# Performance work log

Measured on AMD Instinct MI355X. Metric: run time of the kernel, lower is better.

The kernel has to match this reference:

```python
import jax, jax.numpy as jnp
import numpy as np

N_CLASSES = 19
N_BINS = 10
EPS = 1e-13


def setup_inputs() -> dict:
    key = jax.random.key(0)
    k1, k2 = jax.random.split(key)
    output = jax.random.normal(k1, (1, N_CLASSES, 1024, 2048), dtype=jnp.float32)
    target = jax.random.randint(k2, (1, 1024, 2048), 0, N_CLASSES, dtype=jnp.int32)
    return {"output": output, "target": target}


def reference(output, target):
    # output: [B, C, H, W] logits; target: [B, H, W] int labels
    B, C, H, W = output.shape
    p = jax.nn.softmax(output, axis=1)  # [B, C, H, W]

    # Bin i covers (i/N_BINS, (i+1)/N_BINS]; p == 0 belongs to no bin.
    bin_idx = jnp.clip(jnp.ceil(p * N_BINS).astype(jnp.int32) - 1, 0, N_BINS - 1)
    valid = p > 0

    cls = jnp.arange(C, dtype=jnp.int32)[None, :, None, None]  # idealMap per class
    # Combined (class, bin) segment id; invalid pixels dumped into extra segment.
    seg = jnp.where(valid, cls * N_BINS + bin_idx, C * N_BINS).reshape(-1)
    n_seg = C * N_BINS + 1

    p_flat = p.reshape(-1)
    conf_sum = jax.ops.segment_sum(p_flat, seg, num_segments=n_seg)[:-1].reshape(C, N_BINS)
    no_pred = jax.ops.segment_sum(jnp.ones_like(p_flat), seg, num_segments=n_seg)[:-1].reshape(C, N_BINS)
    correct = (target[:, None, :, :] == cls).astype(p.dtype)  # idealMap == target
    no_acc = jax.ops.segment_sum(correct.reshape(-1), seg, num_segments=n_seg)[:-1].reshape(C, N_BINS)

    avg_acc = no_acc / (no_pred + EPS)
    avg_conf = conf_sum / (no_pred + EPS)
    loss = jnp.sum((avg_acc - avg_conf) ** 2 * (no_pred / jnp.sum(no_pred)))
    return loss
```

## Files before the change

### kernel.cpp

```cpp
#include <hip/hip_runtime.h>

#define NC 19
#define NB 10
#define NCELL (NC * NB)
#define NPART (3 * NCELL + 2 * NC)
#define REP 16
#define NSLOT 32
#define TPB 256
#define BLOCKS 768

typedef float f32x4 __attribute__((ext_vector_type(4)));

__global__ __launch_bounds__(TPB, 3) void cce_pass1(
    const float* __restrict__ logits, const int* __restrict__ tgt,
    float* __restrict__ gacc, int hw)
{
    constexpr int O_CONF = 0;
    constexpr int O_PRED = REP * NCELL;
    constexpr int O_ACC  = 2 * REP * NCELL;
    constexpr int O_PSUM = 3 * REP * NCELL;
    constexpr int O_INV  = O_PSUM + REP * NC;
    constexpr int LDS_N  = O_INV + NC;

    __shared__ float hist[LDS_N];
    for (int i = threadIdx.x; i < LDS_N; i += TPB) hist[i] = 0.0f;
    __syncthreads();

    const int rep = threadIdx.x & (REP - 1);
    float psum[NC];
#pragma unroll
    for (int c = 0; c < NC; ++c) psum[c] = 0.0f;

    const int ngr      = hw >> 2;
    const int tid      = blockIdx.x * TPB + threadIdx.x;
    const int nthreads = (int)gridDim.x * TPB;

    for (int g = tid; g < ngr; g += nthreads) {
        const unsigned voff = (unsigned)g * 16u;
        f32x4 xv[19];
#define LD(i) asm volatile("global_load_dwordx4 %0, %1, %2"                      \
                           : "=v"(xv[i])                                          \
                           : "v"(voff), "s"(logits + (size_t)(i) * hw));
        LD(0) LD(1) LD(2) LD(3) LD(4) LD(5) LD(6) LD(7) LD(8) LD(9)
        LD(10) LD(11) LD(12) LD(13) LD(14) LD(15) LD(16) LD(17) LD(18)
#undef LD
        const int4 tq = *reinterpret_cast<const int4*>(tgt + 4 * (size_t)g);
        asm volatile("s_waitcnt vmcnt(0)"
                     : "+v"(xv[0]), "+v"(xv[1]), "+v"(xv[2]), "+v"(xv[3]),
                       "+v"(xv[4]), "+v"(xv[5]), "+v"(xv[6]), "+v"(xv[7]),
                       "+v"(xv[8]), "+v"(xv[9]), "+v"(xv[10]), "+v"(xv[11]),
                       "+v"(xv[12]), "+v"(xv[13]), "+v"(xv[14]), "+v"(xv[15]),
                       "+v"(xv[16]), "+v"(xv[17]), "+v"(xv[18])
                     :: "memory");

#pragma unroll
        for (int k = 0; k < 4; ++k) {
            const int tgk = (k == 0) ? tq.x : (k == 1) ? tq.y : (k == 2) ? tq.z : tq.w;

            float m = xv[0][k];
#pragma unroll
            for (int c = 1; c < NC; ++c) m = fmaxf(m, xv[c][k]);
            float s = 0.0f;
#pragma unroll
            for (int c = 0; c < NC; ++c) { xv[c][k] = __expf(xv[c][k] - m); s += xv[c][k]; }
            const float r = __builtin_amdgcn_rcpf(s);

            float pt = 0.0f, pmin = 1.0f;
#pragma unroll
            for (int c = 0; c < NC; ++c) {
                const float p = xv[c][k] * r;
                psum[c] += p;
                pt   = (c == tgk) ? p : pt;
                pmin = fminf(pmin, p);
                int bb = (int)ceilf(p * 10.0f) - 1;
                if (bb > 0) {
                    bb = bb > NB - 1 ? NB - 1 : bb;
                    atomicAdd(&hist[O_CONF + rep * NCELL + c * NB + bb], p);
                    atomicAdd(&hist[O_PRED + rep * NCELL + c * NB + bb], 1.0f);
                }
            }
            if (pt > 0.0f) {
                int bt = (int)ceilf(pt * 10.0f) - 1;
                bt = bt < 0 ? 0 : (bt > NB - 1 ? NB - 1 : bt);
                atomicAdd(&hist[O_ACC + rep * NCELL + tgk * NB + bt], 1.0f);
            }
            if (!(pmin > 0.0f)) {
#pragma unroll
                for (int c = 0; c < NC; ++c)
                    if (!(xv[c][k] * r > 0.0f)) atomicAdd(&hist[O_INV + c], 1.0f);
            }
        }
    }

#pragma unroll
    for (int c = 0; c < NC; ++c)
        atomicAdd(&hist[O_PSUM + rep * NC + c], psum[c]);
    __syncthreads();

    float* slot = gacc + (size_t)(blockIdx.x & (NSLOT - 1)) * NPART;
    for (int j = threadIdx.x; j < NPART; j += TPB) {
        float v = 0.0f;
        if (j < NCELL) {
            for (int rr = 0; rr < REP; ++rr) v += hist[O_CONF + rr * NCELL + j];
        } else if (j < 2 * NCELL) {
            for (int rr = 0; rr < REP; ++rr) v += hist[O_PRED + rr * NCELL + (j - NCELL)];
        } else if (j < 3 * NCELL) {
            for (int rr = 0; rr < REP; ++rr) v += hist[O_ACC + rr * NCELL + (j - 2 * NCELL)];
        } else if (j < 3 * NCELL + NC) {
            for (int rr = 0; rr < REP; ++rr) v += hist[O_PSUM + rr * NC + (j - 3 * NCELL)];
        } else {
            v = hist[O_INV + (j - 3 * NCELL - NC)];
        }
        atomicAdd(&slot[j], v);
    }
}

__global__ void cce_pass2(const float* __restrict__ gacc, float* __restrict__ out, int hw)
{
    __shared__ double fin[NPART];
    const int j = threadIdx.x;
    if (j < NPART) {
        double v = 0.0;
        for (int s = 0; s < NSLOT; ++s) v += (double)gacc[(size_t)s * NPART + j];
        fin[j] = v;
    }
    __syncthreads();

    if (j < NC) {
        double spred = 0.0, sconf = 0.0;
        for (int b = 1; b < NB; ++b) {
            spred += fin[NCELL + j * NB + b];
            sconf += fin[j * NB + b];
        }
        const double validc = (double)hw - fin[3 * NCELL + NC + j];
        fin[NCELL + j * NB] = validc - spred;
        fin[j * NB]         = fin[3 * NCELL + j] - sconf;
    }
    __syncthreads();

    if (j < 64) {
        double tot = 0.0;
        for (int c = j; c < NCELL; c += 64) tot += fin[NCELL + c];
#pragma unroll
        for (int o = 32; o > 0; o >>= 1) tot += __shfl_down(tot, o);
        tot = __shfl(tot, 0);

        double loss = 0.0;
        for (int c = j; c < NCELL; c += 64) {
            const double pred = fin[NCELL + c];
            const double conf = fin[c];
            const double acc  = fin[2 * NCELL + c];
            const double d    = (acc - conf) / (pred + 1e-13);
            loss += d * d * (pred / tot);
        }
#pragma unroll
        for (int o = 32; o > 0; o >>= 1) loss += __shfl_down(loss, o);
        if (j == 0) out[0] = (float)loss;
    }
}

extern "C" void kernel_launch(void* const* d_in, const int* in_sizes, int n_in,
                              void* d_out, int out_size, void* d_ws, size_t ws_size,
                              hipStream_t stream)
{
    const float* logits = (const float*)d_in[0];
    const int*   tgt    = (const int*)d_in[1];
    float*       gacc   = (float*)d_ws;
    const int    hw     = in_sizes[1];

    hipMemsetAsync(gacc, 0, (size_t)NSLOT * NPART * sizeof(float), stream);
    cce_pass1<<<BLOCKS, TPB, 0, stream>>>(logits, tgt, gacc, hw);
    cce_pass2<<<1, 640, 0, stream>>>(gacc, (float*)d_out, hw);
}
```

Measured before the change: 267.7 us.

## Process fixed 8-pixel chunk per thread with three-pass streaming softmax

Replaces the grid-stride loop, which held all 19 class vectors in registers, with a one-shot layout: each block covers 2048 pixels and each thread 8 pixels. The thread reads the logits three times (max, sum of exponentials, then histogram), relying on cache hits for the second and third reads so that fewer registers are live. Occupancy rises to 4 blocks per CU, and the LDS histogram replicas drop from 16 to 4 to save shared memory, which adds atomic contention. The grid is hardcoded to 1024 blocks with no bounds check, so the kernel only works when hw is exactly 1024*2048.

```diff
diff --git a/kernel.cpp b/kernel.cpp
--- a/kernel.cpp
+++ b/kernel.cpp
@@ -4,14 +4,16 @@
 #define NB 10
 #define NCELL (NC * NB)
 #define NPART (3 * NCELL + 2 * NC)
-#define REP 16
+#define REP 4
+#define REP16 16
 #define NSLOT 32
 #define TPB 256
-#define BLOCKS 768
+#define CHUNK 2048
+#define BLOCKS 1024
 
 typedef float f32x4 __attribute__((ext_vector_type(4)));
 
-__global__ __launch_bounds__(TPB, 3) void cce_pass1(
+__global__ __launch_bounds__(TPB, 4) void cce_pass1(
     const float* __restrict__ logits, const int* __restrict__ tgt,
     float* __restrict__ gacc, int hw)
 {
@@ -19,82 +21,88 @@
     constexpr int O_PRED = REP * NCELL;
     constexpr int O_ACC  = 2 * REP * NCELL;
     constexpr int O_PSUM = 3 * REP * NCELL;
-    constexpr int O_INV  = O_PSUM + REP * NC;
+    constexpr int O_INV  = O_PSUM + REP16 * NC;
     constexpr int LDS_N  = O_INV + NC;
 
     __shared__ float hist[LDS_N];
     for (int i = threadIdx.x; i < LDS_N; i += TPB) hist[i] = 0.0f;
     __syncthreads();
 
-    const int rep = threadIdx.x & (REP - 1);
-    float psum[NC];
+    const int rep   = threadIdx.x & (REP - 1);
+    const int rep16 = threadIdx.x & (REP16 - 1);
+    const size_t px0 = (size_t)blockIdx.x * CHUNK + (size_t)threadIdx.x * 8;
+
+    int tg[8];
+    {
+        const int4 t0 = *reinterpret_cast<const int4*>(tgt + px0);
+        const int4 t1 = *reinterpret_cast<const int4*>(tgt + px0 + 4);
+        tg[0]=t0.x; tg[1]=t0.y; tg[2]=t0.z; tg[3]=t0.w;
+        tg[4]=t1.x; tg[5]=t1.y; tg[6]=t1.z; tg[7]=t1.w;
+    }
+
+    float m[8];
 #pragma unroll
-    for (int c = 0; c < NC; ++c) psum[c] = 0.0f;
-
-    const int ngr      = hw >> 2;
-    const int tid      = blockIdx.x * TPB + threadIdx.x;
-    const int nthreads = (int)gridDim.x * TPB;
-
-    for (int g = tid; g < ngr; g += nthreads) {
-        const unsigned voff = (unsigned)g * 16u;
-        f32x4 xv[19];
-#define LD(i) asm volatile("global_load_dwordx4 %0, %1, %2"                      \
-                           : "=v"(xv[i])                                          \
-                           : "v"(voff), "s"(logits + (size_t)(i) * hw));
-        LD(0) LD(1) LD(2) LD(3) LD(4) LD(5) LD(6) LD(7) LD(8) LD(9)
-        LD(10) LD(11) LD(12) LD(13) LD(14) LD(15) LD(16) LD(17) LD(18)
-#undef LD
-        const int4 tq = *reinterpret_cast<const int4*>(tgt + 4 * (size_t)g);
-        asm volatile("s_waitcnt vmcnt(0)"
-                     : "+v"(xv[0]), "+v"(xv[1]), "+v"(xv[2]), "+v"(xv[3]),
-                       "+v"(xv[4]), "+v"(xv[5]), "+v"(xv[6]), "+v"(xv[7]),
-                       "+v"(xv[8]), "+v"(xv[9]), "+v"(xv[10]), "+v"(xv[11]),
-                       "+v"(xv[12]), "+v"(xv[13]), "+v"(xv[14]), "+v"(xv[15]),
-                       "+v"(xv[16]), "+v"(xv[17]), "+v"(xv[18])
-                     :: "memory");
-
+    for (int j = 0; j < 8; ++j) m[j] = -1e30f;
 #pragma unroll
-        for (int k = 0; k < 4; ++k) {
-            const int tgk = (k == 0) ? tq.x : (k == 1) ? tq.y : (k == 2) ? tq.z : tq.w;
-
-            float m = xv[0][k];
+    for (int c = 0; c < NC; ++c) {
+        const float* pl = logits + (size_t)c * hw + px0;
+        const f32x4 a = *reinterpret_cast<const f32x4*>(pl);
+        const f32x4 b = *reinterpret_cast<const f32x4*>(pl + 4);
 #pragma unroll
-            for (int c = 1; c < NC; ++c) m = fmaxf(m, xv[c][k]);
-            float s = 0.0f;
-#pragma unroll
-            for (int c = 0; c < NC; ++c) { xv[c][k] = __expf(xv[c][k] - m); s += xv[c][k]; }
-            const float r = __builtin_amdgcn_rcpf(s);
-
-            float pt = 0.0f, pmin = 1.0f;
-#pragma unroll
-            for (int c = 0; c < NC; ++c) {
-                const float p = xv[c][k] * r;
-                psum[c] += p;
-                pt   = (c == tgk) ? p : pt;
-                pmin = fminf(pmin, p);
-                int bb = (int)ceilf(p * 10.0f) - 1;
-                if (bb > 0) {
-                    bb = bb > NB - 1 ? NB - 1 : bb;
-                    atomicAdd(&hist[O_CONF + rep * NCELL + c * NB + bb], p);
-                    atomicAdd(&hist[O_PRED + rep * NCELL + c * NB + bb], 1.0f);
-                }
-            }
-            if (pt > 0.0f) {
-                int bt = (int)ceilf(pt * 10.0f) - 1;
-                bt = bt < 0 ? 0 : (bt > NB - 1 ? NB - 1 : bt);
-                atomicAdd(&hist[O_ACC + rep * NCELL + tgk * NB + bt], 1.0f);
-            }
-            if (!(pmin > 0.0f)) {
-#pragma unroll
-                for (int c = 0; c < NC; ++c)
-                    if (!(xv[c][k] * r > 0.0f)) atomicAdd(&hist[O_INV + c], 1.0f);
-            }
+        for (int j = 0; j < 4; ++j) {
+            m[j]     = fmaxf(m[j],     a[j]);
+            m[4 + j] = fmaxf(m[4 + j], b[j]);
         }
     }
 
+    float S[8];
 #pragma unroll
-    for (int c = 0; c < NC; ++c)
-        atomicAdd(&hist[O_PSUM + rep * NC + c], psum[c]);
+    for (int j = 0; j < 8; ++j) S[j] = 0.0f;
+#pragma unroll
+    for (int c = 0; c < NC; ++c) {
+        const float* pl = logits + (size_t)c * hw + px0;
+        const f32x4 a = *reinterpret_cast<const f32x4*>(pl);
+        const f32x4 b = *reinterpret_cast<const f32x4*>(pl + 4);
+#pragma unroll
+        for (int j = 0; j < 4; ++j) {
+            S[j]     += __expf(a[j] - m[j]);
+            S[4 + j] += __expf(b[j] - m[4 + j]);
+        }
+    }
+    float rc[8];
+#pragma unroll
+    for (int j = 0; j < 8; ++j) rc[j] = __builtin_amdgcn_rcpf(S[j]);
+
+#pragma unroll
+    for (int c = 0; c < NC; ++c) {
+        const float* pl = logits + (size_t)c * hw + px0;
+        const f32x4 a = *reinterpret_cast<const f32x4*>(pl);
+        const f32x4 b = *reinterpret_cast<const f32x4*>(pl + 4);
+        float x[8];
+#pragma unroll
+        for (int j = 0; j < 4; ++j) { x[j] = a[j]; x[4 + j] = b[j]; }
+
+        float ps = 0.0f;
+#pragma unroll
+        for (int j = 0; j < 8; ++j) {
+            const float p = __expf(x[j] - m[j]) * rc[j];
+            ps += p;
+            int bb = (int)ceilf(p * 10.0f) - 1;
+            if (bb > 0) {
+                bb = bb > NB - 1 ? NB - 1 : bb;
+                atomicAdd(&hist[O_CONF + rep * NCELL + c * NB + bb], p);
+                atomicAdd(&hist[O_PRED + rep * NCELL + c * NB + bb], 1.0f);
+            }
+            if (tg[j] == c && p > 0.0f) {
+                int bt = (int)ceilf(p * 10.0f) - 1;
+                bt = bt < 0 ? 0 : (bt > NB - 1 ? NB - 1 : bt);
+                atomicAdd(&hist[O_ACC + rep * NCELL + c * NB + bt], 1.0f);
+            }
+            if (!(p > 0.0f))
+                atomicAdd(&hist[O_INV + c], 1.0f);
+        }
+        atomicAdd(&hist[O_PSUM + rep16 * NC + c], ps);
+    }
     __syncthreads();
 
     float* slot = gacc + (size_t)(blockIdx.x & (NSLOT - 1)) * NPART;
@@ -107,7 +115,7 @@
         } else if (j < 3 * NCELL) {
             for (int rr = 0; rr < REP; ++rr) v += hist[O_ACC + rr * NCELL + (j - 2 * NCELL)];
         } else if (j < 3 * NCELL + NC) {
-            for (int rr = 0; rr < REP; ++rr) v += hist[O_PSUM + rr * NC + (j - 3 * NCELL)];
+            for (int rr = 0; rr < REP16; ++rr) v += hist[O_PSUM + rr * NC + (j - 3 * NCELL)];
         } else {
             v = hist[O_INV + (j - 3 * NCELL - NC)];
         }
```

Result: slower. 359.3 us (+34.2%).
